# Optimization experiments

Measured on AMD Instinct MI355X. Metric: run time of the kernel, lower is better.

The kernel has to match this reference:

```python
import jax, jax.numpy as jnp
import numpy as np

SIMS = 16
AMP = 1.0  # cfg['attention_amplifier']


def setup_inputs() -> dict:
    key = jax.random.key(0)
    k1, k2, k3 = jax.random.split(key, 3)
    B, F = 32, 2048
    data = jax.random.normal(k1, (B * SIMS, F), dtype=jnp.float32)
    attention = jax.random.normal(k2, (B * SIMS, F), dtype=jnp.float32)
    W = jax.random.normal(k3, (SIMS, 2 * SIMS), dtype=jnp.float32) * (1.0 / np.sqrt(2 * SIMS))
    b = jnp.zeros((SIMS,), dtype=jnp.float32)
    return {"data": data, "attention": attention, "W": W, "b": b}


def reference(data, attention, W, b):
    s = SIMS
    B = data.shape[0] // s
    inputs = data.reshape(B, s, -1)            # [B, s, F]
    attn_in = attention.reshape(B, s, -1)      # [B, s, G]
    # bmm(inputs^T, attention) -> [B, F, G]
    a = jnp.einsum('bsf,bsg->bfg', inputs, attn_in)
    a = jax.nn.log_softmax(a, axis=1)          # log_softmax over F dim (dim=1)
    # bmm(a, attention^T) -> [B, F, s]
    a = jnp.einsum('bfg,bsg->bfs', a, attn_in)
    concat = jnp.concatenate([jnp.swapaxes(a, 1, 2), inputs], axis=1)  # [B, 2s, F]
    concat = jnp.swapaxes(concat, 1, 2).reshape(-1, 2 * s)             # [B*F, 2s]
    gate = jax.nn.sigmoid(concat @ W.T + b)    # [B*F, s]
    # output.t().contiguous().view(data.shape): [s, B*F] row-major -> [B*s, F]
    gate = gate.T.reshape(data.shape)
    return gate * data * AMP
```

## Files before the change

kernel.cpp:

```cpp
#include <hip/hip_runtime.h>
#include <math.h>

#define LOG2E 1.44269504088896340736f
#define LN2   0.69314718055994530942f

typedef _Float16 half8 __attribute__((ext_vector_type(8)));
typedef float f32x4v __attribute__((ext_vector_type(4)));

#define AROW 24

template <bool ATOMIC>
__global__ __launch_bounds__(256, 4) void kA(const float* __restrict__ data,
                                             const float* __restrict__ attn,
                                             float* __restrict__ Lout) {
    __shared__ _Float16 AhB[128 * AROW];
    __shared__ _Float16 AlB[128 * AROW];
    const int tid = threadIdx.x;
    const int b = blockIdx.z, fb = blockIdx.y, gb = blockIdx.x;
    const int wave = tid >> 6, lane = tid & 63;
    const int n = lane & 15, q = lane >> 4;
    const int s0 = (q & 1) * 8;

    const float* Tb = attn + (size_t)b * 16 * 2048;
    half8 B1[2], B2[2];
#pragma unroll
    for (int ct = 0; ct < 2; ++ct) {
        const int g = gb * 128 + wave * 32 + ct * 16 + n;
        half8 bh, bl;
#pragma unroll
        for (int j = 0; j < 8; ++j) {
            float x = Tb[(size_t)(s0 + j) * 2048 + g] * LOG2E;
            _Float16 h = (_Float16)x;
            _Float16 l = (_Float16)(x - (float)h);
            bh[j] = h;
            bl[j] = (q < 2) ? l : (_Float16)0.0f;
        }
        B1[ct] = bh;
        B2[ct] = bl;
    }

    f32x4v cs0 = {0.f, 0.f, 0.f, 0.f}, cs1 = {0.f, 0.f, 0.f, 0.f};

    const float* Ab = data + (size_t)b * 16 * 2048 + fb * 512;
    const int fst = tid & 127;
    const int sh  = (tid >> 7) * 8;
    const _Float16* aptr = ((q < 2) ? AhB : AlB) + n * AROW + s0;

    for (int chunk = 0; chunk < 4; ++chunk) {
        const float* Ac = Ab + chunk * 128;
        _Float16 hb[8], lb[8];
#pragma unroll
        for (int j = 0; j < 8; ++j) {
            float x = Ac[(size_t)(sh + j) * 2048 + fst];
            _Float16 h = (_Float16)x;
            hb[j] = h;
            lb[j] = (_Float16)(x - (float)h);
        }
        __syncthreads();
        half8 hv, lv;
#pragma unroll
        for (int j = 0; j < 8; ++j) { hv[j] = hb[j]; lv[j] = lb[j]; }
        *(half8*)(AhB + fst * AROW + sh) = hv;
        *(half8*)(AlB + fst * AROW + sh) = lv;
        __syncthreads();

#pragma unroll
        for (int rt = 0; rt < 8; ++rt) {
            half8 af = *(const half8*)(aptr + rt * 16 * AROW);
            f32x4v C = {0.f, 0.f, 0.f, 0.f};
            C = __builtin_amdgcn_mfma_f32_16x16x32_f16(af, B1[0], C, 0, 0, 0);
            C = __builtin_amdgcn_mfma_f32_16x16x32_f16(af, B2[0], C, 0, 0, 0);
            cs0[0] += __builtin_amdgcn_exp2f(C[0]);
            cs0[1] += __builtin_amdgcn_exp2f(C[1]);
            cs0[2] += __builtin_amdgcn_exp2f(C[2]);
            cs0[3] += __builtin_amdgcn_exp2f(C[3]);
            f32x4v D = {0.f, 0.f, 0.f, 0.f};
            D = __builtin_amdgcn_mfma_f32_16x16x32_f16(af, B1[1], D, 0, 0, 0);
            D = __builtin_amdgcn_mfma_f32_16x16x32_f16(af, B2[1], D, 0, 0, 0);
            cs1[0] += __builtin_amdgcn_exp2f(D[0]);
            cs1[1] += __builtin_amdgcn_exp2f(D[1]);
            cs1[2] += __builtin_amdgcn_exp2f(D[2]);
            cs1[3] += __builtin_amdgcn_exp2f(D[3]);
        }
    }

    float v0 = cs0[0] + cs0[1] + cs0[2] + cs0[3];
    float v1 = cs1[0] + cs1[1] + cs1[2] + cs1[3];
    v0 += __shfl_xor(v0, 16);
    v0 += __shfl_xor(v0, 32);
    v1 += __shfl_xor(v1, 16);
    v1 += __shfl_xor(v1, 32);
    if (q == 0) {
        const int g = gb * 128 + wave * 32 + n;
        if (ATOMIC) {
            atomicAdd(&Lout[(size_t)b * 2048 + g], v0);
            atomicAdd(&Lout[(size_t)b * 2048 + g + 16], v1);
        } else {
            Lout[((size_t)fb * 32 + b) * 2048 + g] = v0;
            Lout[((size_t)fb * 32 + b) * 2048 + g + 16] = v1;
        }
    }
}

#define TP 260
__global__ __launch_bounds__(256) void kTail(const float* __restrict__ attn,
                                             const float* __restrict__ Lpart, int nparts,
                                             float* __restrict__ Mpart,
                                             float* __restrict__ cpart) {
    __shared__ float Tsh[16 * TP];
    __shared__ float Lsh[256];
    __shared__ float red[16][17];
    const int tid = threadIdx.x;
    const int seg = blockIdx.x, b = blockIdx.y;
    const int g0 = seg * 256;

#pragma unroll
    for (int s = 0; s < 16; ++s)
        Tsh[s * TP + tid] = attn[(size_t)(b * 16 + s) * 2048 + g0 + tid];
    {
        float sum = 0.f;
        for (int p = 0; p < nparts; ++p)
            sum += Lpart[((size_t)p * 32 + b) * 2048 + g0 + tid];
        Lsh[tid] = LN2 * __builtin_amdgcn_logf(sum);
    }
    __syncthreads();

    {
        const int t = tid & 15, i = tid >> 4;
        float acc = 0.f;
#pragma unroll
        for (int k = 0; k < 4; ++k) {
            float4 l  = *(const float4*)(Lsh + i * 16 + k * 4);
            float4 tv = *(const float4*)(Tsh + t * TP + i * 16 + k * 4);
            acc += l.x * tv.x + l.y * tv.y + l.z * tv.z + l.w * tv.w;
        }
        red[t][i] = acc;
    }
    __syncthreads();
    if (tid < 16) {
        float s = 0.f;
#pragma unroll
        for (int k = 0; k < 16; ++k) s += red[tid][k];
        cpart[((size_t)seg * 32 + b) * 16 + tid] = s;
    }

    {
        const int s = tid >> 4, t = tid & 15;
        float a0 = 0.f, a1 = 0.f;
#pragma unroll 4
        for (int qk = 0; qk < 32; ++qk) {
            float4 x = *(const float4*)(Tsh + s * TP + qk * 8);
            float4 y = *(const float4*)(Tsh + t * TP + qk * 8);
            a0 += x.x * y.x + x.y * y.y + x.z * y.z + x.w * y.w;
            float4 x2 = *(const float4*)(Tsh + s * TP + qk * 8 + 4);
            float4 y2 = *(const float4*)(Tsh + t * TP + qk * 8 + 4);
            a1 += x2.x * y2.x + x2.y * y2.y + x2.z * y2.z + x2.w * y2.w;
        }
        Mpart[((size_t)seg * 32 + b) * 256 + tid] = a0 + a1;
    }
}

__global__ __launch_bounds__(256) void kC2(const float* __restrict__ data,
                                           const float* __restrict__ Mpart,
                                           const float* __restrict__ cpart,
                                           const float* __restrict__ W,
                                           const float* __restrict__ bias,
                                           float* __restrict__ out) {
    __shared__ float Msh[256];
    __shared__ float csh[16];
    __shared__ float Vsh[256];
    __shared__ float w0sh[16];
    const int tid = threadIdx.x;
    const int b = blockIdx.y;
    const int f = blockIdx.x * 256 + tid;

    {
        float m = 0.f;
#pragma unroll
        for (int p = 0; p < 8; ++p) m += Mpart[((size_t)p * 32 + b) * 256 + tid];
        Msh[tid] = m;
        if (tid < 16) {
            float c = 0.f;
#pragma unroll
            for (int p = 0; p < 8; ++p) c += cpart[((size_t)p * 32 + b) * 16 + tid];
            csh[tid] = c;
        }
    }
    __syncthreads();
    {
        const int s = tid >> 4, j = tid & 15;
        float acc = 0.f;
#pragma unroll
        for (int t = 0; t < 16; ++t) acc += Msh[s * 16 + t] * W[j * 32 + t];
        Vsh[s * 16 + j] = acc + W[j * 32 + 16 + s];
        if (s == 0) {
            float w0 = 0.f;
#pragma unroll
            for (int t = 0; t < 16; ++t) w0 += csh[t] * W[j * 32 + t];
            w0sh[j] = bias[j] - w0;
        }
    }
    __syncthreads();

    float As[16];
#pragma unroll
    for (int s = 0; s < 16; ++s)
        As[s] = data[(size_t)(b * 16 + s) * 2048 + f];
#pragma unroll
    for (int j = 0; j < 16; ++j) {
        float p = w0sh[j];
#pragma unroll
        for (int s = 0; s < 16; ++s) p += As[s] * Vsh[s * 16 + j];
        float e = __builtin_amdgcn_exp2f(-LOG2E * p);
        float gate = __builtin_amdgcn_rcpf(1.0f + e);
        size_t r = (size_t)(j * 32 + b) * 2048 + f;
        out[r] = gate * data[r];
    }
}

extern "C" void kernel_launch(void* const* d_in, const int* in_sizes, int n_in,
                              void* d_out, int out_size, void* d_ws, size_t ws_size,
                              hipStream_t stream) {
    const float* data = (const float*)d_in[0];
    const float* attn = (const float*)d_in[1];
    const float* W    = (const float*)d_in[2];
    const float* bias = (const float*)d_in[3];
    float* out = (float*)d_out;
    float* ws  = (float*)d_ws;

    const size_t LP = 4 * 32 * 2048;
    const size_t need_big = LP + 65536 + 4096;

    if (ws_size >= need_big * sizeof(float)) {
        float* Lpart = ws;
        float* Mpart = ws + LP;
        float* cpart = Mpart + 65536;
        kA<false><<<dim3(16, 4, 32), 256, 0, stream>>>(data, attn, Lpart);
        kTail<<<dim3(8, 32), 256, 0, stream>>>(attn, Lpart, 4, Mpart, cpart);
        kC2<<<dim3(8, 32), 256, 0, stream>>>(data, Mpart, cpart, W, bias, out);
    } else {
        float* Lsum  = ws;
        float* Mpart = ws + 65536;
        float* cpart = Mpart + 65536;
        hipMemsetAsync(Lsum, 0, 65536 * sizeof(float), stream);
        kA<true><<<dim3(16, 4, 32), 256, 0, stream>>>(data, attn, Lsum);
        kTail<<<dim3(8, 32), 256, 0, stream>>>(attn, Lsum, 1, Mpart, cpart);
        kC2<<<dim3(8, 32), 256, 0, stream>>>(data, Mpart, cpart, W, bias, out);
    }
}
```

Baseline: 95.23 us.

## Double-buffer LDS tiles in kA and halve the F-split across blocks

The column-sum kernel now double-buffers the fp16 hi/lo split tiles in shared memory. It prefetches the next 128-column chunk of data into registers while the MFMAs run on the current one, which leaves one barrier per chunk instead of two. Each block also covers 1024 F columns (8 chunks) instead of 512, so the grid's F dimension halves and the tail kernel reduces 2 partials instead of 4. The trade-offs are twice the LDS, more registers, and half as many blocks, which may lower occupancy and parallelism.

```diff
diff --git a/kernel.cpp b/kernel.cpp
--- a/kernel.cpp
+++ b/kernel.cpp
@@ -13,8 +13,8 @@
 __global__ __launch_bounds__(256, 4) void kA(const float* __restrict__ data,
                                              const float* __restrict__ attn,
                                              float* __restrict__ Lout) {
-    __shared__ _Float16 AhB[128 * AROW];
-    __shared__ _Float16 AlB[128 * AROW];
+    __shared__ _Float16 AhB[2][128 * AROW];
+    __shared__ _Float16 AlB[2][128 * AROW];
     const int tid = threadIdx.x;
     const int b = blockIdx.z, fb = blockIdx.y, gb = blockIdx.x;
     const int wave = tid >> 6, lane = tid & 63;
@@ -41,29 +41,37 @@
 
     f32x4v cs0 = {0.f, 0.f, 0.f, 0.f}, cs1 = {0.f, 0.f, 0.f, 0.f};
 
-    const float* Ab = data + (size_t)b * 16 * 2048 + fb * 512;
+    const float* Ab = data + (size_t)b * 16 * 2048 + fb * 1024;
     const int fst = tid & 127;
     const int sh  = (tid >> 7) * 8;
-    const _Float16* aptr = ((q < 2) ? AhB : AlB) + n * AROW + s0;
-
-    for (int chunk = 0; chunk < 4; ++chunk) {
-        const float* Ac = Ab + chunk * 128;
-        _Float16 hb[8], lb[8];
+
+    {
+        float x[8];
+#pragma unroll
+        for (int j = 0; j < 8; ++j) x[j] = Ab[(size_t)(sh + j) * 2048 + fst];
+        half8 hv, lv;
 #pragma unroll
         for (int j = 0; j < 8; ++j) {
-            float x = Ac[(size_t)(sh + j) * 2048 + fst];
-            _Float16 h = (_Float16)x;
-            hb[j] = h;
-            lb[j] = (_Float16)(x - (float)h);
-        }
-        __syncthreads();
-        half8 hv, lv;
-#pragma unroll
-        for (int j = 0; j < 8; ++j) { hv[j] = hb[j]; lv[j] = lb[j]; }
-        *(half8*)(AhB + fst * AROW + sh) = hv;
-        *(half8*)(AlB + fst * AROW + sh) = lv;
-        __syncthreads();
-
+            _Float16 h = (_Float16)x[j];
+            hv[j] = h;
+            lv[j] = (_Float16)(x[j] - (float)h);
+        }
+        *(half8*)(&AhB[0][fst * AROW + sh]) = hv;
+        *(half8*)(&AlB[0][fst * AROW + sh]) = lv;
+    }
+    __syncthreads();
+
+#pragma unroll 2
+    for (int c = 0; c < 8; ++c) {
+        const int cur = c & 1;
+        float xn[8];
+        if (c < 7) {
+            const float* Ac = Ab + (c + 1) * 128;
+#pragma unroll
+            for (int j = 0; j < 8; ++j) xn[j] = Ac[(size_t)(sh + j) * 2048 + fst];
+        }
+
+        const _Float16* aptr = ((q < 2) ? AhB[cur] : AlB[cur]) + n * AROW + s0;
 #pragma unroll
         for (int rt = 0; rt < 8; ++rt) {
             half8 af = *(const half8*)(aptr + rt * 16 * AROW);
@@ -82,6 +90,20 @@
             cs1[2] += __builtin_amdgcn_exp2f(D[2]);
             cs1[3] += __builtin_amdgcn_exp2f(D[3]);
         }
+
+        if (c < 7) {
+            half8 hv, lv;
+#pragma unroll
+            for (int j = 0; j < 8; ++j) {
+                _Float16 h = (_Float16)xn[j];
+                hv[j] = h;
+                lv[j] = (_Float16)(xn[j] - (float)h);
+            }
+            const int nxt = cur ^ 1;
+            *(half8*)(&AhB[nxt][fst * AROW + sh]) = hv;
+            *(half8*)(&AlB[nxt][fst * AROW + sh]) = lv;
+            __syncthreads();
+        }
     }
 
     float v0 = cs0[0] + cs0[1] + cs0[2] + cs0[3];
@@ -228,22 +250,22 @@
     float* out = (float*)d_out;
     float* ws  = (float*)d_ws;
 
-    const size_t LP = 4 * 32 * 2048;
+    const size_t LP = 2 * 32 * 2048;
     const size_t need_big = LP + 65536 + 4096;
 
     if (ws_size >= need_big * sizeof(float)) {
         float* Lpart = ws;
         float* Mpart = ws + LP;
         float* cpart = Mpart + 65536;
-        kA<false><<<dim3(16, 4, 32), 256, 0, stream>>>(data, attn, Lpart);
-        kTail<<<dim3(8, 32), 256, 0, stream>>>(attn, Lpart, 4, Mpart, cpart);
+        kA<false><<<dim3(16, 2, 32), 256, 0, stream>>>(data, attn, Lpart);
+        kTail<<<dim3(8, 32), 256, 0, stream>>>(attn, Lpart, 2, Mpart, cpart);
         kC2<<<dim3(8, 32), 256, 0, stream>>>(data, Mpart, cpart, W, bias, out);
     } else {
         float* Lsum  = ws;
         float* Mpart = ws + 65536;
         float* cpart = Mpart + 65536;
         hipMemsetAsync(Lsum, 0, 65536 * sizeof(float), stream);
-        kA<true><<<dim3(16, 4, 32), 256, 0, stream>>>(data, attn, Lsum);
+        kA<true><<<dim3(16, 2, 32), 256, 0, stream>>>(data, attn, Lsum);
         kTail<<<dim3(8, 32), 256, 0, stream>>>(attn, Lsum, 1, Mpart, cpart);
         kC2<<<dim3(8, 32), 256, 0, stream>>>(data, Mpart, cpart, W, bias, out);
     }
```

Measured after the change: 197.3 us. 107% more time.
